# Kernel tuning notes

Hardware: AMD Instinct MI355X
Metric: run time of the kernel (lower is better)

## Reference

```python
import jax, jax.numpy as jnp
import numpy as np
from jax import lax

DIM = 384
NUM_HEADS = 12
HEAD_DIM = DIM // NUM_HEADS
SCALE = HEAD_DIM ** -0.5


def setup_inputs() -> dict:
    key = jax.random.key(0)
    ks = jax.random.split(key, 7)
    B, H, W = 8, 32, 32
    s = 0.02
    return {
        "x": jax.random.normal(ks[0], (B, DIM, H, W), jnp.float32),
        "qkvo_w": jax.random.normal(ks[1], (4 * DIM, DIM, 1, 1), jnp.float32) * s,
        "qkvo_b": jax.random.normal(ks[2], (4 * DIM,), jnp.float32) * s,
        "lepe_w": jax.random.normal(ks[3], (DIM, 1, 5, 5), jnp.float32) * s,
        "lepe_b": jax.random.normal(ks[4], (DIM,), jnp.float32) * s,
        "proj_w": jax.random.normal(ks[5], (DIM, DIM, 1, 1), jnp.float32) * s,
        "proj_b": jax.random.normal(ks[6], (DIM,), jnp.float32) * s,
    }


def reference(x, qkvo_w, qkvo_b, lepe_w, lepe_b, proj_w, proj_b):
    B, C, H, W = x.shape
    n, d = NUM_HEADS, HEAD_DIM
    HW = H * W

    # fused 1x1 QKVO projection: [B, 4C, H, W]
    qkvo = jnp.einsum('oc,bchw->bohw', qkvo_w[:, :, 0, 0], x) + qkvo_b[:, None, None]
    qkv = qkvo[:, :3 * C]
    o = qkvo[:, 3 * C:]

    # depthwise 5x5 LePE on v channels
    v_ch = qkv[:, 2 * C:]
    lepe = lax.conv_general_dilated(
        v_ch, lepe_w, window_strides=(1, 1), padding='SAME',
        feature_group_count=C,
        dimension_numbers=('NCHW', 'OIHW', 'NCHW')) + lepe_b[:, None, None]

    # split heads: channels ordered (m n d) -> q,k,v each [B, n, HW, d]
    q, k, v = jnp.transpose(qkv.reshape(B, 3, n, d, HW), (1, 0, 2, 4, 3))

    attn = jax.nn.softmax(SCALE * jnp.einsum('bnqd,bnkd->bnqk', q, k), axis=-1)
    res = jnp.einsum('bnqk,bnkd->bnqd', attn, v)  # [B, n, HW, d]
    res = jnp.transpose(res, (0, 1, 3, 2)).reshape(B, C, H, W)

    res = res + lepe
    out = jnp.einsum('oc,bchw->bohw', proj_w[:, :, 0, 0], res * o) + proj_b[:, None, None]
    return out
```

## Files before the change

kernel.cpp:

```cpp
#include <hip/hip_runtime.h>
#include <hip/hip_bf16.h>

#define DIM   384
#define NH    12
#define HD    32
#define HWSZ  1024
#define BATCH 8
#define SCALE 0.17677669529663687f
#define EXP_K (SCALE * 1.4426950408889634f)

typedef __attribute__((ext_vector_type(8))) short bf16x8;
typedef __attribute__((ext_vector_type(4))) float floatx4;

__device__ __forceinline__ unsigned short f2bf(float x) {
    union { __hip_bfloat16 h; unsigned short u; } c;
    c.h = __float2bfloat16(x);
    return c.u;
}
__device__ __forceinline__ float bf2f(unsigned short h) {
    union { unsigned int u; float f; } v; v.u = ((unsigned int)h) << 16;
    return v.f;
}

__global__ __launch_bounds__(256) void cast_w(
    const float* __restrict__ wa, const float* __restrict__ wb,
    unsigned short* __restrict__ da, unsigned short* __restrict__ db, int na8)
{
    const int idx = blockIdx.x * 256 + threadIdx.x;
    const float* src; unsigned short* dst; int i;
    if (idx < na8) { src = wa; dst = da; i = idx; }
    else           { src = wb; dst = db; i = idx - na8; }
    float4 f0 = *(const float4*)&src[i * 8];
    float4 f1 = *(const float4*)&src[i * 8 + 4];
    ushort4 h0 = make_ushort4(f2bf(f0.x), f2bf(f0.y), f2bf(f0.z), f2bf(f0.w));
    ushort4 h1 = make_ushort4(f2bf(f1.x), f2bf(f1.y), f2bf(f1.z), f2bf(f1.w));
    *(ushort4*)&dst[i * 8] = h0;
    *(ushort4*)&dst[i * 8 + 4] = h1;
}

__global__ __launch_bounds__(256) void tcast_f32(
    const float* __restrict__ in, unsigned short* __restrict__ out, int C, int N)
{
    __shared__ __align__(16) unsigned short t[32][36];
    const int n0 = blockIdx.x * 32, c0 = blockIdx.y * 32, b = blockIdx.z;
    const float* ib = in + (size_t)b * C * N;
    unsigned short* ob = out + (size_t)b * N * C;
    const int tid = threadIdx.x;
    const int r = tid >> 3, q = (tid & 7) * 4;
    float4 f = *(const float4*)&ib[(size_t)(c0 + r) * N + n0 + q];
    ushort4 h = make_ushort4(f2bf(f.x), f2bf(f.y), f2bf(f.z), f2bf(f.w));
    *(ushort4*)&t[r][q] = h;
    __syncthreads();
    ushort4 o;
    o.x = t[q + 0][r]; o.y = t[q + 1][r]; o.z = t[q + 2][r]; o.w = t[q + 3][r];
    *(ushort4*)&ob[(size_t)(n0 + r) * C + c0 + q] = o;
}

__global__ __launch_bounds__(256) void tcast_b16(
    const unsigned short* __restrict__ in, unsigned short* __restrict__ out, int C, int N)
{
    __shared__ __align__(16) unsigned short t[32][36];
    const int n0 = blockIdx.x * 32, c0 = blockIdx.y * 32, b = blockIdx.z;
    const unsigned short* ib = in + (size_t)b * C * N;
    unsigned short* ob = out + (size_t)b * N * C;
    const int tid = threadIdx.x;
    const int r = tid >> 3, q = (tid & 7) * 4;
    ushort4 h = *(const ushort4*)&ib[(size_t)(c0 + r) * N + n0 + q];
    *(ushort4*)&t[r][q] = h;
    __syncthreads();
    ushort4 o;
    o.x = t[q + 0][r]; o.y = t[q + 1][r]; o.z = t[q + 2][r]; o.w = t[q + 3][r];
    *(ushort4*)&ob[(size_t)(n0 + r) * C + c0 + q] = o;
}

template<int MODE>
__global__ __launch_bounds__(256) void gemm_mfma(
    const unsigned short* __restrict__ Wb16, const unsigned short* __restrict__ Xt,
    const float* __restrict__ bias, unsigned short* __restrict__ qkT,
    unsigned short* __restrict__ vo, float* __restrict__ Yf,
    int M, int K, int N)
{
    __shared__ __align__(16) unsigned short lds[16896];
    #define AS(r, k) lds[(r) * 40 + (k)]
    #define BS(r, k) lds[5120 + (r) * 40 + (k)]
    #define CS(r, c2) lds[(r) * 132 + (c2)]

    const int b = blockIdx.z, m0 = blockIdx.y * 128, n0 = blockIdx.x * 128;
    const int tid = threadIdx.x;
    const int w = tid >> 6, lane = tid & 63;
    const int wr = w >> 1, wc = w & 1;
    const int g = lane >> 4, c = lane & 15;

    const bool SWAPPED = (MODE == 0) && (m0 >= 768);

    const unsigned short* Xb = Xt + (size_t)b * N * K;

    floatx4 acc[4][4];
    #pragma unroll
    for (int i = 0; i < 4; ++i)
        #pragma unroll
        for (int j = 0; j < 4; ++j) acc[i][j] = (floatx4){0.f, 0.f, 0.f, 0.f};

    const int srow = tid >> 1, shh = (tid & 1) * 16;

    for (int k0 = 0; k0 < K; k0 += 32) {
        __syncthreads();
        {
            const unsigned short* wp = &Wb16[(size_t)(m0 + srow) * K + k0 + shh];
            *(bf16x8*)&AS(srow, shh)     = *(const bf16x8*)wp;
            *(bf16x8*)&AS(srow, shh + 8) = *(const bf16x8*)(wp + 8);
            const unsigned short* xp = &Xb[(size_t)(n0 + srow) * K + k0 + shh];
            *(bf16x8*)&BS(srow, shh)     = *(const bf16x8*)xp;
            *(bf16x8*)&BS(srow, shh + 8) = *(const bf16x8*)(xp + 8);
        }
        __syncthreads();

        bf16x8 af[4], bfj[4];
        #pragma unroll
        for (int i = 0; i < 4; ++i)
            af[i] = *(const bf16x8*)&AS(64 * wr + 16 * i + c, 8 * g);
        #pragma unroll
        for (int j = 0; j < 4; ++j)
            bfj[j] = *(const bf16x8*)&BS(64 * wc + 16 * j + c, 8 * g);
        if (!SWAPPED) {
            #pragma unroll
            for (int i = 0; i < 4; ++i)
                #pragma unroll
                for (int j = 0; j < 4; ++j)
                    acc[i][j] = __builtin_amdgcn_mfma_f32_16x16x32_bf16(
                        af[i], bfj[j], acc[i][j], 0, 0, 0);
        } else {
            #pragma unroll
            for (int i = 0; i < 4; ++i)
                #pragma unroll
                for (int j = 0; j < 4; ++j)
                    acc[i][j] = __builtin_amdgcn_mfma_f32_16x16x32_bf16(
                        bfj[j], af[i], acc[i][j], 0, 0, 0);
        }
    }

    if (MODE == 1) {
        #pragma unroll
        for (int i = 0; i < 4; ++i) {
            const int m = m0 + 64 * wr + 16 * i + 4 * g;
            float bi[4];
            #pragma unroll
            for (int r = 0; r < 4; ++r) bi[r] = bias[m + r];
            #pragma unroll
            for (int j = 0; j < 4; ++j) {
                const int n = n0 + 64 * wc + 16 * j + c;
                #pragma unroll
                for (int r = 0; r < 4; ++r)
                    Yf[((size_t)b * M + m + r) * (size_t)N + n] = acc[i][j][r] + bi[r];
            }
        }
        return;
    }

    __syncthreads();

    if (m0 < 768) {
        const float qs = (m0 < 384) ? EXP_K : 1.0f;
        #pragma unroll
        for (int i = 0; i < 4; ++i) {
            const int mb = 64 * wr + 16 * i + 4 * g;
            float bi[4];
            #pragma unroll
            for (int r = 0; r < 4; ++r) bi[r] = bias[m0 + mb + r];
            #pragma unroll
            for (int j = 0; j < 4; ++j) {
                const int nl = 64 * wc + 16 * j + c;
                ushort4 h;
                h.x = f2bf((acc[i][j][0] + bi[0]) * qs);
                h.y = f2bf((acc[i][j][1] + bi[1]) * qs);
                h.z = f2bf((acc[i][j][2] + bi[2]) * qs);
                h.w = f2bf((acc[i][j][3] + bi[3]) * qs);
                *(ushort4*)&CS(nl, mb) = h;
            }
        }
        __syncthreads();
        const int rl = tid >> 1, half = (tid & 1) * 64;
        unsigned short* dst = &qkT[((size_t)b * HWSZ + n0 + rl) * 768 + m0 + half];
        const unsigned short* src = &CS(rl, half);
        #pragma unroll
        for (int u = 0; u < 8; ++u)
            *(bf16x8*)(dst + 8 * u) = *(const bf16x8*)(src + 8 * u);
    } else {
        #pragma unroll
        for (int i = 0; i < 4; ++i) {
            const int ml = 64 * wr + 16 * i + c;
            const float bi = bias[m0 + ml];
            #pragma unroll
            for (int j = 0; j < 4; ++j) {
                const int nb = 64 * wc + 16 * j + 4 * g;
                ushort4 h;
                h.x = f2bf(acc[i][j][0] + bi);
                h.y = f2bf(acc[i][j][1] + bi);
                h.z = f2bf(acc[i][j][2] + bi);
                h.w = f2bf(acc[i][j][3] + bi);
                *(ushort4*)&CS(ml, nb) = h;
            }
        }
        __syncthreads();
        const int rl = tid >> 1, half = (tid & 1) * 64;
        unsigned short* dst =
            &vo[((size_t)b * 768 + (m0 - 768) + rl) * HWSZ + n0 + half];
        const unsigned short* src = &CS(rl, half);
        #pragma unroll
        for (int u = 0; u < 8; ++u)
            *(bf16x8*)(dst + 8 * u) = *(const bf16x8*)(src + 8 * u);
    }
    #undef AS
    #undef BS
    #undef CS
}

__global__ __launch_bounds__(512) void attn_mfma(
    const unsigned short* __restrict__ qkT, const unsigned short* __restrict__ vo,
    unsigned short* __restrict__ res)
{
    __shared__ __align__(16) unsigned short Ks[64][40];
    __shared__ __align__(16) unsigned short Vs[32][72];
    __shared__ __align__(16) unsigned short Ps[128][72];
    __shared__ float lbuf[128];

    const int b = blockIdx.z, h = blockIdx.y, p0 = blockIdx.x * 128;
    const int tid = threadIdx.x;
    const int w = tid >> 6, lane = tid & 63;
    const int g = lane >> 4, c = lane & 15;

    const unsigned short* qkTb = qkT + (size_t)b * HWSZ * 768;
    const unsigned short* vb   = vo + ((size_t)b * 768 + h * HD) * HWSZ;

    bf16x8 qf = *(const bf16x8*)&qkTb[(size_t)(p0 + 16 * w + c) * 768 + h * HD + 8 * g];

    floatx4 oacc0 = (floatx4){0.f, 0.f, 0.f, 0.f};
    floatx4 oacc1 = (floatx4){0.f, 0.f, 0.f, 0.f};
    float Lacc = 0.f;

    for (int j0 = 0; j0 < HWSZ; j0 += 64) {
        __syncthreads();
        if (tid < 256) {
            const int jr = tid >> 2, d8 = (tid & 3) * 8;
            *(bf16x8*)&Ks[jr][d8] =
                *(const bf16x8*)&qkTb[(size_t)(j0 + jr) * 768 + 384 + h * HD + d8];
        } else {
            const int t = tid - 256;
            const int dr = t >> 3, j8 = (t & 7) * 8;
            *(bf16x8*)&Vs[dr][j8] =
                *(const bf16x8*)&vb[(size_t)dr * HWSZ + j0 + j8];
        }
        __syncthreads();

        #pragma unroll
        for (int jb = 0; jb < 4; ++jb) {
            bf16x8 kf = *(const bf16x8*)&Ks[jb * 16 + c][8 * g];
            floatx4 st = (floatx4){0.f, 0.f, 0.f, 0.f};
            st = __builtin_amdgcn_mfma_f32_16x16x32_bf16(kf, qf, st, 0, 0, 0);
            float e0 = exp2f(st[0]);
            float e1 = exp2f(st[1]);
            float e2 = exp2f(st[2]);
            float e3 = exp2f(st[3]);
            Lacc += (e0 + e1) + (e2 + e3);
            ushort4 pe = make_ushort4(f2bf(e0), f2bf(e1), f2bf(e2), f2bf(e3));
            *(ushort4*)&Ps[16 * w + c][jb * 16 + 4 * g] = pe;
        }

        #pragma unroll
        for (int jk = 0; jk < 2; ++jk) {
            bf16x8 pf  = *(const bf16x8*)&Ps[16 * w + c][jk * 32 + 8 * g];
            bf16x8 vf0 = *(const bf16x8*)&Vs[c][jk * 32 + 8 * g];
            bf16x8 vf1 = *(const bf16x8*)&Vs[16 + c][jk * 32 + 8 * g];
            oacc0 = __builtin_amdgcn_mfma_f32_16x16x32_bf16(pf, vf0, oacc0, 0, 0, 0);
            oacc1 = __builtin_amdgcn_mfma_f32_16x16x32_bf16(pf, vf1, oacc1, 0, 0, 0);
        }
    }

    Lacc += __shfl_xor(Lacc, 16, 64);
    Lacc += __shfl_xor(Lacc, 32, 64);
    if (g == 0) lbuf[16 * w + c] = Lacc;

    float linv[4];
    #pragma unroll
    for (int r = 0; r < 4; ++r) linv[r] = 1.0f / lbuf[16 * w + 4 * g + r];

    unsigned short* rp = res + ((size_t)b * DIM + h * HD) * HWSZ;
    const int pbase = p0 + 16 * w + 4 * g;
    ushort4 h0, h1;
    h0.x = f2bf(oacc0[0] * linv[0]); h0.y = f2bf(oacc0[1] * linv[1]);
    h0.z = f2bf(oacc0[2] * linv[2]); h0.w = f2bf(oacc0[3] * linv[3]);
    h1.x = f2bf(oacc1[0] * linv[0]); h1.y = f2bf(oacc1[1] * linv[1]);
    h1.z = f2bf(oacc1[2] * linv[2]); h1.w = f2bf(oacc1[3] * linv[3]);
    *(ushort4*)&rp[(size_t)c * HWSZ + pbase] = h0;
    *(ushort4*)&rp[(size_t)(16 + c) * HWSZ + pbase] = h1;
}

__global__ __launch_bounds__(256) void lepe_mul(
    const unsigned short* __restrict__ vo, const float* __restrict__ lw,
    const float* __restrict__ lb, const unsigned short* __restrict__ res,
    unsigned short* __restrict__ gated)
{
    const int cch = blockIdx.x, b = blockIdx.y;
    const unsigned short* v  = vo + ((size_t)b * 768 + cch) * HWSZ;
    const unsigned short* o  = vo + ((size_t)b * 768 + 384 + cch) * HWSZ;
    const unsigned short* rp = res + ((size_t)b * DIM + cch) * HWSZ;
    unsigned short* gp = gated + ((size_t)b * DIM + cch) * HWSZ;

    __shared__ float vs[1024];
    __shared__ float wgt[25];

    const int tid = threadIdx.x;
    {
        ushort4 hv = *(const ushort4*)&v[tid * 4];
        vs[tid * 4 + 0] = bf2f(hv.x); vs[tid * 4 + 1] = bf2f(hv.y);
        vs[tid * 4 + 2] = bf2f(hv.z); vs[tid * 4 + 3] = bf2f(hv.w);
    }
    if (tid < 25) wgt[tid] = lw[cch * 25 + tid];
    __syncthreads();

    const float bias = lb[cch];
    const int q0 = tid * 4;
    const int y  = q0 >> 5;
    const int x0 = q0 & 31;

    float acc[4] = {bias, bias, bias, bias};
    #pragma unroll
    for (int ky = 0; ky < 5; ++ky) {
        int iy = y + ky - 2;
        if ((unsigned)iy < 32u) {
            #pragma unroll
            for (int kx = 0; kx < 5; ++kx) {
                float wv = wgt[ky * 5 + kx];
                #pragma unroll
                for (int u = 0; u < 4; ++u) {
                    int ix = x0 + u + kx - 2;
                    if ((unsigned)ix < 32u) acc[u] += wv * vs[iy * 32 + ix];
                }
            }
        }
    }

    ushort4 rh = *(const ushort4*)&rp[q0];
    ushort4 oh = *(const ushort4*)&o[q0];
    ushort4 outv;
    outv.x = f2bf((bf2f(rh.x) + acc[0]) * bf2f(oh.x));
    outv.y = f2bf((bf2f(rh.y) + acc[1]) * bf2f(oh.y));
    outv.z = f2bf((bf2f(rh.z) + acc[2]) * bf2f(oh.z));
    outv.w = f2bf((bf2f(rh.w) + acc[3]) * bf2f(oh.w));
    *(ushort4*)&gp[q0] = outv;
}

extern "C" void kernel_launch(void* const* d_in, const int* in_sizes, int n_in,
                              void* d_out, int out_size, void* d_ws, size_t ws_size,
                              hipStream_t stream)
{
    const float* x      = (const float*)d_in[0];
    const float* qkvo_w = (const float*)d_in[1];
    const float* qkvo_b = (const float*)d_in[2];
    const float* lepe_w = (const float*)d_in[3];
    const float* lepe_b = (const float*)d_in[4];
    const float* proj_w = (const float*)d_in[5];
    const float* proj_b = (const float*)d_in[6];

    unsigned short* xt     = (unsigned short*)d_ws;
    unsigned short* qkT    = xt     + (size_t)BATCH * HWSZ * DIM;
    unsigned short* vo     = qkT    + (size_t)BATCH * HWSZ * 768;
    unsigned short* res    = vo     + (size_t)BATCH * 768 * HWSZ;
    unsigned short* gated  = res    + (size_t)BATCH * DIM * HWSZ;
    unsigned short* gatedT = gated  + (size_t)BATCH * DIM * HWSZ;
    unsigned short* wqb    = gatedT + (size_t)BATCH * HWSZ * DIM;
    unsigned short* wpb    = wqb    + (size_t)1536 * DIM;

    cast_w<<<dim3((73728 + 18432) / 256), 256, 0, stream>>>(
        qkvo_w, proj_w, wqb, wpb, 73728);

    tcast_f32<<<dim3(32, 12, BATCH), 256, 0, stream>>>(x, xt, DIM, HWSZ);

    gemm_mfma<0><<<dim3(8, 12, BATCH), 256, 0, stream>>>(
        wqb, xt, qkvo_b, qkT, vo, nullptr, 4 * DIM, DIM, HWSZ);

    attn_mfma<<<dim3(8, NH, BATCH), 512, 0, stream>>>(qkT, vo, res);

    lepe_mul<<<dim3(DIM, BATCH), 256, 0, stream>>>(vo, lepe_w, lepe_b, res, gated);

    tcast_b16<<<dim3(32, 12, BATCH), 256, 0, stream>>>(gated, gatedT, DIM, HWSZ);

    gemm_mfma<1><<<dim3(8, 3, BATCH), 256, 0, stream>>>(
        wpb, gatedT, proj_b, nullptr, nullptr, (float*)d_out, DIM, DIM, HWSZ);
}
```

Baseline: 181.7 us.

## Merge prep casts, retile projection GEMM, compute softmax row sums via MFMA

Folds the weight cast and the input transpose-cast into one launch, removing a kernel launch. The projection GEMM gets its own kernel with 64x64 tiles, giving four times as many blocks (768 instead of 192) so it fills the GPU better, at the cost of less reuse per block. In attention, the softmax denominator is now accumulated by an extra MFMA against a ones vector instead of scalar adds, shuffles and an LDS buffer. The sum now uses the bf16-rounded probabilities, which matches the numerator more closely.

```diff
diff --git a/kernel.cpp b/kernel.cpp
--- a/kernel.cpp
+++ b/kernel.cpp
@@ -22,38 +22,38 @@
     return v.f;
 }
 
-__global__ __launch_bounds__(256) void cast_w(
-    const float* __restrict__ wa, const float* __restrict__ wb,
-    unsigned short* __restrict__ da, unsigned short* __restrict__ db, int na8)
-{
-    const int idx = blockIdx.x * 256 + threadIdx.x;
-    const float* src; unsigned short* dst; int i;
-    if (idx < na8) { src = wa; dst = da; i = idx; }
-    else           { src = wb; dst = db; i = idx - na8; }
-    float4 f0 = *(const float4*)&src[i * 8];
-    float4 f1 = *(const float4*)&src[i * 8 + 4];
-    ushort4 h0 = make_ushort4(f2bf(f0.x), f2bf(f0.y), f2bf(f0.z), f2bf(f0.w));
-    ushort4 h1 = make_ushort4(f2bf(f1.x), f2bf(f1.y), f2bf(f1.z), f2bf(f1.w));
-    *(ushort4*)&dst[i * 8] = h0;
-    *(ushort4*)&dst[i * 8 + 4] = h1;
-}
-
-__global__ __launch_bounds__(256) void tcast_f32(
-    const float* __restrict__ in, unsigned short* __restrict__ out, int C, int N)
-{
-    __shared__ __align__(16) unsigned short t[32][36];
-    const int n0 = blockIdx.x * 32, c0 = blockIdx.y * 32, b = blockIdx.z;
-    const float* ib = in + (size_t)b * C * N;
-    unsigned short* ob = out + (size_t)b * N * C;
-    const int tid = threadIdx.x;
-    const int r = tid >> 3, q = (tid & 7) * 4;
-    float4 f = *(const float4*)&ib[(size_t)(c0 + r) * N + n0 + q];
-    ushort4 h = make_ushort4(f2bf(f.x), f2bf(f.y), f2bf(f.z), f2bf(f.w));
-    *(ushort4*)&t[r][q] = h;
-    __syncthreads();
-    ushort4 o;
-    o.x = t[q + 0][r]; o.y = t[q + 1][r]; o.z = t[q + 2][r]; o.w = t[q + 3][r];
-    *(ushort4*)&ob[(size_t)(n0 + r) * C + c0 + q] = o;
+__global__ __launch_bounds__(256) void prep(
+    const float* __restrict__ x, const float* __restrict__ qkvo_w,
+    const float* __restrict__ proj_w, unsigned short* __restrict__ xt,
+    unsigned short* __restrict__ wqb, unsigned short* __restrict__ wpb)
+{
+    const int tid = threadIdx.x;
+    if (blockIdx.z < 8) {
+        __shared__ __align__(16) unsigned short t[32][36];
+        const int n0 = blockIdx.x * 32, c0 = blockIdx.y * 32, b = blockIdx.z;
+        const float* ib = x + (size_t)b * DIM * HWSZ;
+        unsigned short* ob = xt + (size_t)b * HWSZ * DIM;
+        const int r = tid >> 3, q = (tid & 7) * 4;
+        float4 f = *(const float4*)&ib[(size_t)(c0 + r) * HWSZ + n0 + q];
+        ushort4 h = make_ushort4(f2bf(f.x), f2bf(f.y), f2bf(f.z), f2bf(f.w));
+        *(ushort4*)&t[r][q] = h;
+        __syncthreads();
+        ushort4 o;
+        o.x = t[q + 0][r]; o.y = t[q + 1][r]; o.z = t[q + 2][r]; o.w = t[q + 3][r];
+        *(ushort4*)&ob[(size_t)(n0 + r) * DIM + c0 + q] = o;
+    } else {
+        const int idx = (blockIdx.y * 32 + blockIdx.x) * 256 + tid;
+        if (idx >= 92160) return;
+        const float* src; unsigned short* dst; int i;
+        if (idx < 73728) { src = qkvo_w; dst = wqb; i = idx; }
+        else             { src = proj_w; dst = wpb; i = idx - 73728; }
+        float4 f0 = *(const float4*)&src[i * 8];
+        float4 f1 = *(const float4*)&src[i * 8 + 4];
+        ushort4 h0 = make_ushort4(f2bf(f0.x), f2bf(f0.y), f2bf(f0.z), f2bf(f0.w));
+        ushort4 h1 = make_ushort4(f2bf(f1.x), f2bf(f1.y), f2bf(f1.z), f2bf(f1.w));
+        *(ushort4*)&dst[i * 8] = h0;
+        *(ushort4*)&dst[i * 8 + 4] = h1;
+    }
 }
 
 __global__ __launch_bounds__(256) void tcast_b16(
@@ -73,12 +73,10 @@
     *(ushort4*)&ob[(size_t)(n0 + r) * C + c0 + q] = o;
 }
 
-template<int MODE>
-__global__ __launch_bounds__(256) void gemm_mfma(
+__global__ __launch_bounds__(256) void gemm_qkvo(
     const unsigned short* __restrict__ Wb16, const unsigned short* __restrict__ Xt,
     const float* __restrict__ bias, unsigned short* __restrict__ qkT,
-    unsigned short* __restrict__ vo, float* __restrict__ Yf,
-    int M, int K, int N)
+    unsigned short* __restrict__ vo)
 {
     __shared__ __align__(16) unsigned short lds[16896];
     #define AS(r, k) lds[(r) * 40 + (k)]
@@ -90,10 +88,9 @@
     const int w = tid >> 6, lane = tid & 63;
     const int wr = w >> 1, wc = w & 1;
     const int g = lane >> 4, c = lane & 15;
-
-    const bool SWAPPED = (MODE == 0) && (m0 >= 768);
-
-    const unsigned short* Xb = Xt + (size_t)b * N * K;
+    const bool SWAPPED = (m0 >= 768);
+
+    const unsigned short* Xb = Xt + (size_t)b * HWSZ * DIM;
 
     floatx4 acc[4][4];
     #pragma unroll
@@ -103,13 +100,13 @@
 
     const int srow = tid >> 1, shh = (tid & 1) * 16;
 
-    for (int k0 = 0; k0 < K; k0 += 32) {
+    for (int k0 = 0; k0 < DIM; k0 += 32) {
         __syncthreads();
         {
-            const unsigned short* wp = &Wb16[(size_t)(m0 + srow) * K + k0 + shh];
+            const unsigned short* wp = &Wb16[(size_t)(m0 + srow) * DIM + k0 + shh];
             *(bf16x8*)&AS(srow, shh)     = *(const bf16x8*)wp;
             *(bf16x8*)&AS(srow, shh + 8) = *(const bf16x8*)(wp + 8);
-            const unsigned short* xp = &Xb[(size_t)(n0 + srow) * K + k0 + shh];
+            const unsigned short* xp = &Xb[(size_t)(n0 + srow) * DIM + k0 + shh];
             *(bf16x8*)&BS(srow, shh)     = *(const bf16x8*)xp;
             *(bf16x8*)&BS(srow, shh + 8) = *(const bf16x8*)(xp + 8);
         }
@@ -137,24 +134,6 @@
                     acc[i][j] = __builtin_amdgcn_mfma_f32_16x16x32_bf16(
                         bfj[j], af[i], acc[i][j], 0, 0, 0);
         }
-    }
-
-    if (MODE == 1) {
-        #pragma unroll
-        for (int i = 0; i < 4; ++i) {
-            const int m = m0 + 64 * wr + 16 * i + 4 * g;
-            float bi[4];
-            #pragma unroll
-            for (int r = 0; r < 4; ++r) bi[r] = bias[m + r];
-            #pragma unroll
-            for (int j = 0; j < 4; ++j) {
-                const int n = n0 + 64 * wc + 16 * j + c;
-                #pragma unroll
-                for (int r = 0; r < 4; ++r)
-                    Yf[((size_t)b * M + m + r) * (size_t)N + n] = acc[i][j][r] + bi[r];
-            }
-        }
-        return;
     }
 
     __syncthreads();
@@ -215,6 +194,68 @@
     #undef CS
 }
 
+__global__ __launch_bounds__(256) void gemm_proj(
+    const unsigned short* __restrict__ Wb16, const unsigned short* __restrict__ Xt,
+    const float* __restrict__ bias, float* __restrict__ Yf)
+{
+    __shared__ __align__(16) unsigned short As[64][40];
+    __shared__ __align__(16) unsigned short Bs[64][40];
+
+    const int b = blockIdx.z, m0 = blockIdx.y * 64, n0 = blockIdx.x * 64;
+    const int tid = threadIdx.x;
+    const int w = tid >> 6, lane = tid & 63;
+    const int wr = w >> 1, wc = w & 1;
+    const int g = lane >> 4, c = lane & 15;
+
+    const unsigned short* Xb = Xt + (size_t)b * HWSZ * DIM;
+
+    floatx4 acc[2][2];
+    #pragma unroll
+    for (int i = 0; i < 2; ++i)
+        #pragma unroll
+        for (int j = 0; j < 2; ++j) acc[i][j] = (floatx4){0.f, 0.f, 0.f, 0.f};
+
+    const int srow = tid >> 2, sk8 = (tid & 3) * 8;
+
+    for (int k0 = 0; k0 < DIM; k0 += 32) {
+        __syncthreads();
+        *(bf16x8*)&As[srow][sk8] =
+            *(const bf16x8*)&Wb16[(size_t)(m0 + srow) * DIM + k0 + sk8];
+        *(bf16x8*)&Bs[srow][sk8] =
+            *(const bf16x8*)&Xb[(size_t)(n0 + srow) * DIM + k0 + sk8];
+        __syncthreads();
+
+        bf16x8 af[2], bfj[2];
+        #pragma unroll
+        for (int i = 0; i < 2; ++i)
+            af[i] = *(const bf16x8*)&As[32 * wr + 16 * i + c][8 * g];
+        #pragma unroll
+        for (int j = 0; j < 2; ++j)
+            bfj[j] = *(const bf16x8*)&Bs[32 * wc + 16 * j + c][8 * g];
+        #pragma unroll
+        for (int i = 0; i < 2; ++i)
+            #pragma unroll
+            for (int j = 0; j < 2; ++j)
+                acc[i][j] = __builtin_amdgcn_mfma_f32_16x16x32_bf16(
+                    af[i], bfj[j], acc[i][j], 0, 0, 0);
+    }
+
+    #pragma unroll
+    for (int i = 0; i < 2; ++i) {
+        const int m = m0 + 32 * wr + 16 * i + 4 * g;
+        float bi[4];
+        #pragma unroll
+        for (int r = 0; r < 4; ++r) bi[r] = bias[m + r];
+        #pragma unroll
+        for (int j = 0; j < 2; ++j) {
+            const int n = n0 + 32 * wc + 16 * j + c;
+            #pragma unroll
+            for (int r = 0; r < 4; ++r)
+                Yf[((size_t)b * DIM + m + r) * (size_t)HWSZ + n] = acc[i][j][r] + bi[r];
+        }
+    }
+}
+
 __global__ __launch_bounds__(512) void attn_mfma(
     const unsigned short* __restrict__ qkT, const unsigned short* __restrict__ vo,
     unsigned short* __restrict__ res)
@@ -222,7 +263,6 @@
     __shared__ __align__(16) unsigned short Ks[64][40];
     __shared__ __align__(16) unsigned short Vs[32][72];
     __shared__ __align__(16) unsigned short Ps[128][72];
-    __shared__ float lbuf[128];
 
     const int b = blockIdx.z, h = blockIdx.y, p0 = blockIdx.x * 128;
     const int tid = threadIdx.x;
@@ -234,9 +274,12 @@
 
     bf16x8 qf = *(const bf16x8*)&qkTb[(size_t)(p0 + 16 * w + c) * 768 + h * HD + 8 * g];
 
+    const bf16x8 onesf = {0x3F80, 0x3F80, 0x3F80, 0x3F80,
+                          0x3F80, 0x3F80, 0x3F80, 0x3F80};
+
     floatx4 oacc0 = (floatx4){0.f, 0.f, 0.f, 0.f};
     floatx4 oacc1 = (floatx4){0.f, 0.f, 0.f, 0.f};
-    float Lacc = 0.f;
+    floatx4 lacc  = (floatx4){0.f, 0.f, 0.f, 0.f};
 
     for (int j0 = 0; j0 < HWSZ; j0 += 64) {
         __syncthreads();
@@ -257,12 +300,8 @@
             bf16x8 kf = *(const bf16x8*)&Ks[jb * 16 + c][8 * g];
             floatx4 st = (floatx4){0.f, 0.f, 0.f, 0.f};
             st = __builtin_amdgcn_mfma_f32_16x16x32_bf16(kf, qf, st, 0, 0, 0);
-            float e0 = exp2f(st[0]);
-            float e1 = exp2f(st[1]);
-            float e2 = exp2f(st[2]);
-            float e3 = exp2f(st[3]);
-            Lacc += (e0 + e1) + (e2 + e3);
-            ushort4 pe = make_ushort4(f2bf(e0), f2bf(e1), f2bf(e2), f2bf(e3));
+            ushort4 pe = make_ushort4(f2bf(exp2f(st[0])), f2bf(exp2f(st[1])),
+                                      f2bf(exp2f(st[2])), f2bf(exp2f(st[3])));
             *(ushort4*)&Ps[16 * w + c][jb * 16 + 4 * g] = pe;
         }
 
@@ -273,16 +312,13 @@
             bf16x8 vf1 = *(const bf16x8*)&Vs[16 + c][jk * 32 + 8 * g];
             oacc0 = __builtin_amdgcn_mfma_f32_16x16x32_bf16(pf, vf0, oacc0, 0, 0, 0);
             oacc1 = __builtin_amdgcn_mfma_f32_16x16x32_bf16(pf, vf1, oacc1, 0, 0, 0);
-        }
-    }
-
-    Lacc += __shfl_xor(Lacc, 16, 64);
-    Lacc += __shfl_xor(Lacc, 32, 64);
-    if (g == 0) lbuf[16 * w + c] = Lacc;
+            lacc  = __builtin_amdgcn_mfma_f32_16x16x32_bf16(pf, onesf, lacc, 0, 0, 0);
+        }
+    }
 
     float linv[4];
     #pragma unroll
-    for (int r = 0; r < 4; ++r) linv[r] = 1.0f / lbuf[16 * w + 4 * g + r];
+    for (int r = 0; r < 4; ++r) linv[r] = 1.0f / lacc[r];
 
     unsigned short* rp = res + ((size_t)b * DIM + h * HD) * HWSZ;
     const int pbase = p0 + 16 * w + 4 * g;
@@ -371,13 +407,9 @@
     unsigned short* wqb    = gatedT + (size_t)BATCH * HWSZ * DIM;
     unsigned short* wpb    = wqb    + (size_t)1536 * DIM;
 
-    cast_w<<<dim3((73728 + 18432) / 256), 256, 0, stream>>>(
-        qkvo_w, proj_w, wqb, wpb, 73728);
-
-    tcast_f32<<<dim3(32, 12, BATCH), 256, 0, stream>>>(x, xt, DIM, HWSZ);
-
-    gemm_mfma<0><<<dim3(8, 12, BATCH), 256, 0, stream>>>(
-        wqb, xt, qkvo_b, qkT, vo, nullptr, 4 * DIM, DIM, HWSZ);
+    prep<<<dim3(32, 12, 9), 256, 0, stream>>>(x, qkvo_w, proj_w, xt, wqb, wpb);
+
+    gemm_qkvo<<<dim3(8, 12, BATCH), 256, 0, stream>>>(wqb, xt, qkvo_b, qkT, vo);
 
     attn_mfma<<<dim3(8, NH, BATCH), 512, 0, stream>>>(qkT, vo, res);
 
@@ -385,6 +417,5 @@
 
     tcast_b16<<<dim3(32, 12, BATCH), 256, 0, stream>>>(gated, gatedT, DIM, HWSZ);
 
-    gemm_mfma<1><<<dim3(8, 3, BATCH), 256, 0, stream>>>(
-        wpb, gatedT, proj_b, nullptr, nullptr, (float*)d_out, DIM, DIM, HWSZ);
-}
+    gemm_proj<<<dim3(16, 6, BATCH), 256, 0, stream>>>(wpb, gatedT, proj_b, (float*)d_out);
+}
```

Result: faster. 171.3 us (-5.7%).
